# Performance work log

Hardware: AMD Instinct MI355X
Metric: run time of the kernel (lower is better)

The kernel has to match this reference:

```python
import jax, jax.numpy as jnp
import numpy as np

B, L, HIDDEN = 64, 200, 256
HEADS = 8
MAX_WIDTH = 5
EPS = 1e-5  # F.layer_norm default eps


def _ln(x):
    # F.layer_norm with no learned affine
    m = jnp.mean(x, axis=-1, keepdims=True)
    v = jnp.mean((x - m) ** 2, axis=-1, keepdims=True)
    return (x - m) * jax.lax.rsqrt(v + EPS)


def _area_pool(x, max_width, mode):
    # x: [B, H, L, D] -> pooled spans of widths 1..max_width (valid windows),
    # concatenated along the memory axis: M = sum_w (L - w + 1)
    Lx = x.shape[2]
    outs = []
    for w in range(1, max_width + 1):
        # [w, B, H, L-w+1, D] stack of shifted slices (w <= 5, tiny loop)
        win = jnp.stack([x[:, :, i:Lx - w + 1 + i, :] for i in range(w)], axis=0)
        if mode == 'max':
            outs.append(win.max(axis=0))
        elif mode == 'mean':
            outs.append(win.mean(axis=0))
        else:  # 'sum'
            outs.append(win.sum(axis=0))
    return jnp.concatenate(outs, axis=2)


def _mha_area(q_in, k_in, v_in, Wq, bq, Wk, bk, Wv, bv, Wo, bo):
    # per-head size equals hidden_size (key_query_size_hidden = hidden_size)
    Bq, Lq, _ = q_in.shape
    Dh = Wq.shape[1] // HEADS

    def split(x):
        return x.reshape(x.shape[0], x.shape[1], HEADS, Dh).transpose(0, 2, 1, 3)

    q = split(q_in @ Wq + bq)  # [B, H, Lq, Dh]
    k = split(k_in @ Wk + bk)
    v = split(v_in @ Wv + bv)
    k_area = _area_pool(k, MAX_WIDTH, 'max')   # aggr='max' key pooling
    v_area = _area_pool(v, MAX_WIDTH, 'sum')   # values pooled by sum (t2t default)
    scale = jnp.asarray(1.0 / np.sqrt(Dh), q.dtype)
    logits = jnp.einsum('bhqd,bhmd->bhqm', q, k_area) * scale
    attn = jax.nn.softmax(logits, axis=-1)  # dropout inactive at eval
    out = jnp.einsum('bhqm,bhmd->bhqd', attn, v_area)
    out = out.transpose(0, 2, 1, 3).reshape(Bq, Lq, HEADS * Dh)
    return out @ Wo + bo


def setup_inputs() -> dict:
    key = jax.random.key(0)
    ks = jax.random.split(key, 16)
    stdv = 1.0 / np.sqrt(HIDDEN)
    u = lambda k, shp: jax.random.uniform(k, shp, jnp.float32, -stdv, stdv)
    HD = HEADS * HIDDEN  # 2048
    return {
        'A': jax.random.normal(ks[0], (B, L, L), jnp.float32),
        'hidden': jax.random.normal(ks[1], (B, L, HIDDEN), jnp.float32),
        'Wq': u(ks[2], (HIDDEN, HD)), 'bq': u(ks[3], (HD,)),
        'Wk': u(ks[4], (HIDDEN, HD)), 'bk': u(ks[5], (HD,)),
        'Wv': u(ks[6], (HIDDEN, HD)), 'bv': u(ks[7], (HD,)),
        'Wo': u(ks[8], (HD, HIDDEN)), 'bo': u(ks[9], (HIDDEN,)),
        'W1': u(ks[10], (HIDDEN, 4 * HIDDEN)), 'b1': u(ks[11], (4 * HIDDEN,)),
        'W2': u(ks[12], (4 * HIDDEN, HIDDEN)), 'b2': u(ks[13], (HIDDEN,)),
    }


def reference(A, hidden, Wq, bq, Wk, bk, Wv, bv, Wo, bo, W1, b1, W2, b2):
    # step = 1 -> single ATTNCell; A is unused by ATTNCell (matches source)
    attn1 = _mha_area(hidden, hidden, hidden, Wq, bq, Wk, bk, Wv, bv, Wo, bo)
    attn1 = _ln(attn1 + hidden)
    attn2 = _mha_area(attn1, hidden, hidden, Wq, bq, Wk, bk, Wv, bv, Wo, bo)
    attn2 = _ln(attn1 + attn2)  # F.dropout inactive (eval)
    x = jax.nn.relu(attn2 @ W1 + b1) @ W2 + b2
    return _ln(attn2 + x)
```

## Files before the change

kernel.cpp:

```cpp
#include <hip/hip_runtime.h>
#include <hip/hip_bf16.h>
#include <cstdint>
#include <cstddef>

#define BATCH 64
#define LSEQ 200
#define HID 256
#define NH 8
#define DH 256
#define HD (NH*DH)
#define MROWS (BATCH*LSEQ)
#define EPS 1e-5f
#define CSCALE 0.09014195f

typedef unsigned short ushort_t;
typedef __attribute__((ext_vector_type(8))) short bf16x8;
typedef __attribute__((ext_vector_type(8))) unsigned short u16x8;
typedef __attribute__((ext_vector_type(4))) float f32x4;

__device__ __forceinline__ float b2f(ushort_t u) {
    union { unsigned int i; float f; } c; c.i = ((unsigned int)u) << 16; return c.f;
}
__device__ __forceinline__ ushort_t f2b(float f) {
    __hip_bfloat16 h = __float2bfloat16(f);
    union { __hip_bfloat16 h; ushort_t u; } c; c.h = h; return c.u;
}
__device__ __forceinline__ float to_f32(float x) { return x; }
__device__ __forceinline__ float to_f32(ushort_t x) { return b2f(x); }
__device__ __forceinline__ void store_val(float* p, float v) { *p = v; }
__device__ __forceinline__ void store_val(ushort_t* p, float v) { *p = f2b(v); }

__device__ __forceinline__ u16x8 bmax8(u16x8 a, u16x8 b) {
    union U { u16x8 v; __hip_bfloat162 h[4]; };
    U ua, ub, r; ua.v = a; ub.v = b;
    #pragma unroll
    for (int i = 0; i < 4; ++i) r.h[i] = __hmax2(ua.h[i], ub.h[i]);
    return r.v;
}

__device__ __forceinline__ void gll16(const void* g, void* l) {
    __builtin_amdgcn_global_load_lds(
        (const __attribute__((address_space(1))) unsigned int*)g,
        (__attribute__((address_space(3))) unsigned int*)l, 16, 0, 0);
}

template<bool RELU, int OMODE, bool SCALEC>
__global__ __launch_bounds__(256) void gemm_bt(
    const ushort_t* __restrict__ A, const ushort_t* __restrict__ Bt,
    const float* __restrict__ bias, ushort_t* __restrict__ C,
    int M, int N, int K)
{
    __shared__ ushort_t As[128 * 32];
    __shared__ ushort_t Bs[128 * 32];
    const int t = threadIdx.x;
    const int m0 = blockIdx.y * 128, n0 = blockIdx.x * 128;
    const int wave = t >> 6, lane = t & 63;
    const int l15 = lane & 15, lq = lane >> 4;
    const int wr = wave >> 1, wc = wave & 1;

    f32x4 acc[4][4];
    #pragma unroll
    for (int i = 0; i < 4; ++i)
        #pragma unroll
        for (int j = 0; j < 4; ++j) acc[i][j] = (f32x4){0.f, 0.f, 0.f, 0.f};

    for (int k0 = 0; k0 < K; k0 += 32) {
        __syncthreads();
        #pragma unroll
        for (int i = 0; i < 2; ++i) {
            int li = i * 256 + t;
            int ml = li >> 2, cp = li & 3;
            int cg = cp ^ ((ml ^ (ml >> 2)) & 3);
            gll16(A + (size_t)(m0 + ml) * K + k0 + cg * 8, &As[li * 8]);
        }
        #pragma unroll
        for (int i = 0; i < 2; ++i) {
            int li = i * 256 + t;
            int nl = li >> 2, cp = li & 3;
            int cg = cp ^ ((nl ^ (nl >> 2)) & 3);
            gll16(Bt + (size_t)(n0 + nl) * K + k0 + cg * 8, &Bs[li * 8]);
        }
        __syncthreads();
        bf16x8 af[4], bfr[4];
        #pragma unroll
        for (int i = 0; i < 4; ++i) {
            int r = wr * 64 + i * 16 + l15;
            int pc = lq ^ ((r ^ (r >> 2)) & 3);
            af[i] = *(const bf16x8*)&As[r * 32 + pc * 8];
        }
        #pragma unroll
        for (int j = 0; j < 4; ++j) {
            int r = wc * 64 + j * 16 + l15;
            int pc = lq ^ ((r ^ (r >> 2)) & 3);
            bfr[j] = *(const bf16x8*)&Bs[r * 32 + pc * 8];
        }
        #pragma unroll
        for (int i = 0; i < 4; ++i)
            #pragma unroll
            for (int j = 0; j < 4; ++j)
                acc[i][j] = __builtin_amdgcn_mfma_f32_16x16x32_bf16(af[i], bfr[j], acc[i][j], 0, 0, 0);
    }
    if (OMODE == 2) {
        #pragma unroll
        for (int i = 0; i < 4; ++i) {
            int mbase = m0 + wr * 64 + i * 16 + 4 * lq;
            int bb = (int)(((unsigned)mbase * 5243u) >> 20);
            int ll = mbase - bb * 200;
            #pragma unroll
            for (int j = 0; j < 4; ++j) {
                int n = n0 + wc * 64 + j * 16 + l15;
                float bsv = bias[n];
                ushort4 o4;
                o4.x = f2b(acc[i][j][0] + bsv); o4.y = f2b(acc[i][j][1] + bsv);
                o4.z = f2b(acc[i][j][2] + bsv); o4.w = f2b(acc[i][j][3] + bsv);
                size_t addr = ((size_t)(bb * NH + (n >> 8)) * 256 + (n & 255)) * LSEQ + ll;
                *(ushort4*)&C[addr] = o4;
            }
        }
    } else {
        #pragma unroll
        for (int i = 0; i < 4; ++i) {
            #pragma unroll
            for (int e = 0; e < 4; ++e) {
                int m = m0 + wr * 64 + i * 16 + 4 * lq + e;
                #pragma unroll
                for (int j = 0; j < 4; ++j) {
                    int n = n0 + wc * 64 + j * 16 + l15;
                    float v = acc[i][j][e] + bias[n];
                    if (RELU) v = fmaxf(v, 0.f);
                    if (SCALEC) v *= CSCALE;
                    if (OMODE == 1) {
                        int bb = (int)(((unsigned)m * 5243u) >> 20);
                        int ll = m - bb * 200;
                        size_t addr = ((((size_t)(bb * NH + (n >> 8))) * LSEQ + ll) << 8) + (n & 255);
                        C[addr] = f2b(v);
                    } else {
                        C[(size_t)m * N + n] = f2b(v);
                    }
                }
            }
        }
    }
}

__global__ __launch_bounds__(512, 2) void attn_mfma20(
    const ushort_t* __restrict__ Q, const ushort_t* __restrict__ Khm,
    const ushort_t* __restrict__ Vt, ushort_t* __restrict__ O)
{
    const int id = blockIdx.x;
    const int xcd = id & 7, slot_ = id >> 3;
    const int qt = slot_ & 1;
    const int bh = ((slot_ >> 1) << 3) + xcd;
    const int b = bh >> 3, h = bh & 7;
    const int q0 = qt * 128;
    const int t = threadIdx.x;
    const int wave = t >> 6, lane = t & 63;
    const int l15 = lane & 15, lq = lane >> 4;

    __shared__ ushort_t Ks[2 * 64 * 256];
    __shared__ ushort_t Vs[256 * 64];

    const ushort_t* kbh = Khm + (size_t)bh * LSEQ * DH;
    const ushort_t* vtb = Vt + (size_t)bh * DH * LSEQ;
    const ushort_t* qbh = Q + ((size_t)b * LSEQ) * HD + h * DH;
    const int qrow = q0 + wave * 16 + l15;

    bf16x8 qf[8];
    if (qrow < LSEQ) {
        const ushort_t* qp = qbh + (size_t)qrow * HD + 8 * lq;
        #pragma unroll
        for (int g = 0; g < 8; ++g) qf[g] = *(const bf16x8*)(qp + 32 * g);
    } else {
        bf16x8 zf = {0,0,0,0,0,0,0,0};
        #pragma unroll
        for (int g = 0; g < 8; ++g) qf[g] = zf;
    }

    f32x4 oacc[16];
    #pragma unroll
    for (int i = 0; i < 16; ++i) oacc[i] = (f32x4){0.f, 0.f, 0.f, 0.f};
    float l4[4];
    #pragma unroll
    for (int e = 0; e < 4; ++e) l4[e] = 0.f;
    float carry[4];
    #pragma unroll
    for (int e = 0; e < 4; ++e) carry[e] = 0.f;
    float Pagg[4][4];

    const int dc = t & 31, mb = t >> 5;
    const int vd = t >> 1, vh = t & 1;
    const int srow = ((mb >> 2) << 4) + (mb & 3);

    auto kOff = [&](int k4) {
        int m = mb + 16 * k4;
        return m * 256 + ((dc ^ (m & 15)) * 8);
    };

    auto qk = [&](int bo, f32x4* sacc) {
        __builtin_amdgcn_s_setprio(1);
        #pragma unroll
        for (int ms = 0; ms < 4; ++ms) {
            f32x4 s = (f32x4){0.f, 0.f, 0.f, 0.f};
            const int row = ms * 16 + l15;
            #pragma unroll
            for (int g = 0; g < 8; ++g) {
                const int phys = (lq + 4 * g) ^ l15;
                s = __builtin_amdgcn_mfma_f32_16x16x32_bf16(
                        *(const bf16x8*)&Ks[bo + row * 256 + phys * 8], qf[g], s, 0, 0, 0);
            }
            sacc[ms] = s;
        }
        __builtin_amdgcn_s_setprio(0);
    };

    auto smClass = [&](const f32x4* sacc, int cls) {
        float Pc[4][4];
        #pragma unroll
        for (int ms = 0; ms < 4; ++ms)
            #pragma unroll
            for (int e = 0; e < 4; ++e) {
                float pe = __builtin_exp2f(sacc[ms][e]);
                l4[e] += pe;
                Pc[ms][e] = pe;
                Pagg[ms][e] += pe;
            }
        if (cls >= 1) {
            float T[4][4];
            #pragma unroll
            for (int ms = 0; ms < 4; ++ms)
                #pragma unroll
                for (int e = 0; e < 4; ++e) T[ms][e] = Pc[ms][e];
            #pragma unroll
            for (int u = 1; u <= 4; ++u) {
                if (u <= cls) {
                    float up = __shfl(T[3][3], (lane - 16) & 63);
                    #pragma unroll
                    for (int ms = 3; ms >= 0; --ms) {
                        float nv = (ms > 0) ? T[ms - 1][3] : ((lq > 0) ? up : 0.f);
                        T[ms][3] = T[ms][2]; T[ms][2] = T[ms][1]; T[ms][1] = T[ms][0];
                        T[ms][0] = nv;
                    }
                    #pragma unroll
                    for (int ms = 0; ms < 4; ++ms)
                        #pragma unroll
                        for (int e = 0; e < 4; ++e) Pagg[ms][e] += T[ms][e];
                }
            }
        }
        #pragma unroll
        for (int i = 0; i < 4; ++i)
            #pragma unroll
            for (int e = 0; e < 4; ++e)
                if (cls >= 4 + i - e) carry[i] += Pc[3][e];
    };

    auto pv32 = [&](const float P[4][4]) {
        unsigned int w[8];
        #pragma unroll
        for (int ms = 0; ms < 4; ++ms) {
            asm("v_cvt_pk_bf16_f32 %0, %1, %2" : "=v"(w[2*ms])   : "v"(P[ms][0]), "v"(P[ms][1]));
            asm("v_cvt_pk_bf16_f32 %0, %1, %2" : "=v"(w[2*ms+1]) : "v"(P[ms][2]), "v"(P[ms][3]));
        }
        union FR { unsigned int u[4]; bf16x8 v; };
        FR f0, f1;
        f0.u[0] = w[0]; f0.u[1] = w[1]; f0.u[2] = w[2]; f0.u[3] = w[3];
        f1.u[0] = w[4]; f1.u[1] = w[5]; f1.u[2] = w[6]; f1.u[3] = w[7];
        const bf16x8 pf0 = f0.v, pf1 = f1.v;
        __builtin_amdgcn_s_setprio(1);
        #pragma unroll
        for (int dt = 0; dt < 16; ++dt) {
            const int d = dt * 16 + l15;
            const int p0 = lq ^ (d & 7);
            const int p1 = (lq + 4) ^ (d & 7);
            oacc[dt] = __builtin_amdgcn_mfma_f32_16x16x32_bf16(
                           pf0, *(const bf16x8*)&Vs[d * 64 + p0 * 8], oacc[dt], 0, 0, 0);
            oacc[dt] = __builtin_amdgcn_mfma_f32_16x16x32_bf16(
                           pf1, *(const bf16x8*)&Vs[d * 64 + p1 * 8], oacc[dt], 0, 0, 0);
        }
        __builtin_amdgcn_s_setprio(0);
    };

    auto storeVchunk = [&](int kc, u16x8 val) {
        *(u16x8*)&Vs[vd * 64 + ((kc ^ (vd & 7)) * 8)] = val;
    };

    {
        u16x8 r0[4], r1[4], vc[4];
        #pragma unroll
        for (int k4 = 0; k4 < 4; ++k4) {
            const int s = srow + 4 * k4;
            r0[k4] = *(const u16x8*)(kbh + (size_t)(s) * DH + dc * 8);
            r1[k4] = *(const u16x8*)(kbh + (size_t)(s + 1) * DH + dc * 8);
        }
        const ushort_t* vrow = vtb + (size_t)vd * LSEQ + vh * 32;
        #pragma unroll
        for (int cl = 0; cl < 4; ++cl) vc[cl] = *(const u16x8*)(vrow + cl * 8);
        #pragma unroll
        for (int k4 = 0; k4 < 4; ++k4) {
            const int off = kOff(k4);
            *(u16x8*)&Ks[off] = r0[k4];
            *(u16x8*)&Ks[16384 + off] = bmax8(r0[k4], r1[k4]);
        }
        #pragma unroll
        for (int cl = 0; cl < 4; ++cl) {
            const int cg = vh * 4 + cl;
            storeVchunk((cg & 1) * 4 + (cg >> 1), vc[cl]);
        }
    }
    __syncthreads();

    for (int ti = 0; ti < 3; ++ti) {
        const int st0 = ti * 64;
        {
            float pin0 = __shfl(carry[0], (lane + 48) & 63);
            float pin1 = __shfl(carry[1], (lane + 48) & 63);
            float pin2 = __shfl(carry[2], (lane + 48) & 63);
            float pin3 = __shfl(carry[3], (lane + 48) & 63);
            #pragma unroll
            for (int ms = 0; ms < 4; ++ms)
                #pragma unroll
                for (int e = 0; e < 4; ++e) Pagg[ms][e] = 0.f;
            if (lq == 0) {
                Pagg[0][0] = pin0; Pagg[0][1] = pin1; Pagg[0][2] = pin2; Pagg[0][3] = pin3;
            }
            #pragma unroll
            for (int e = 0; e < 4; ++e) carry[e] = 0.f;
        }
        {
            f32x4 sa[4], sb[4];
            qk(0, sa); qk(16384, sb);
            smClass(sa, 0); smClass(sb, 1);
        }
        {
            u16x8 r2[4], r3[4];
            #pragma unroll
            for (int k4 = 0; k4 < 4; ++k4) {
                const int s = st0 + srow + 4 * k4;
                r2[k4] = *(const u16x8*)(kbh + (size_t)(s + 2) * DH + dc * 8);
                r3[k4] = *(const u16x8*)(kbh + (size_t)(s + 3) * DH + dc * 8);
            }
            __syncthreads();
            #pragma unroll
            for (int k4 = 0; k4 < 4; ++k4) {
                const int off = kOff(k4);
                u16x8 c2 = bmax8(*(const u16x8*)&Ks[16384 + off], r2[k4]);
                *(u16x8*)&Ks[off] = c2;
                *(u16x8*)&Ks[16384 + off] = bmax8(c2, r3[k4]);
            }
            __syncthreads();
        }
        {
            f32x4 sa[4], sb[4];
            qk(0, sa); qk(16384, sb);
            smClass(sa, 2); smClass(sb, 3);
        }
        {
            u16x8 r4[4];
            #pragma unroll
            for (int k4 = 0; k4 < 4; ++k4) {
                const int s = st0 + srow + 4 * k4;
                r4[k4] = *(const u16x8*)(kbh + (size_t)(s + 4) * DH + dc * 8);
            }
            __syncthreads();
            #pragma unroll
            for (int k4 = 0; k4 < 4; ++k4) {
                const int off = kOff(k4);
                *(u16x8*)&Ks[off] = bmax8(*(const u16x8*)&Ks[16384 + off], r4[k4]);
            }
            __syncthreads();
        }
        {
            f32x4 sa[4];
            qk(0, sa);
            smClass(sa, 4);
            pv32(Pagg);
        }
        if (ti < 2) {
            const int nt0 = st0 + 64;
            u16x8 r0[4], r1[4], vc[4];
            #pragma unroll
            for (int k4 = 0; k4 < 4; ++k4) {
                const int s = nt0 + srow + 4 * k4;
                r0[k4] = *(const u16x8*)(kbh + (size_t)(s) * DH + dc * 8);
                r1[k4] = *(const u16x8*)(kbh + (size_t)(s + 1) * DH + dc * 8);
            }
            const ushort_t* vrow = vtb + (size_t)vd * LSEQ + nt0 + vh * 32;
            #pragma unroll
            for (int cl = 0; cl < 4; ++cl) vc[cl] = *(const u16x8*)(vrow + cl * 8);
            __syncthreads();
            #pragma unroll
            for (int k4 = 0; k4 < 4; ++k4) {
                const int off = kOff(k4);
                *(u16x8*)&Ks[off] = r0[k4];
                *(u16x8*)&Ks[16384 + off] = bmax8(r0[k4], r1[k4]);
            }
            #pragma unroll
            for (int cl = 0; cl < 4; ++cl) {
                const int cg = vh * 4 + cl;
                storeVchunk((cg & 1) * 4 + (cg >> 1), vc[cl]);
            }
            __syncthreads();
        } else {
            u16x8 v0 = *(const u16x8*)(vtb + (size_t)vd * LSEQ + 192);
            __syncthreads();
            if (mb < 8) {
                u16x8 krun = *(const u16x8*)(kbh + (size_t)(192 + mb) * DH + dc * 8);
                const u16x8 kz = {0,0,0,0,0,0,0,0};
                #pragma unroll
                for (int k8 = 0; k8 < 8; ++k8) {
                    const bool vv = (k8 <= 4) && (mb <= 7 - k8);
                    if (k8 > 0 && vv)
                        krun = bmax8(krun, *(const u16x8*)(kbh + (size_t)(192 + mb + k8) * DH + dc * 8));
                    int slot = k8 * 8 + mb;
                    *(u16x8*)&Ks[slot * 256 + ((dc ^ (slot & 15)) * 8)] = vv ? krun : kz;
                }
            }
            {
                float f[8];
                #pragma unroll
                for (int e = 0; e < 8; ++e) f[e] = b2f(v0[e]);
                #pragma unroll
                for (int ck = 0; ck < 4; ++ck) {
                    const int kc = vh * 4 + ck;
                    const int cls_lo = 4 * (kc >> 2) + ((kc >> 1) & 1);
                    const int offb = 4 * (kc & 1);
                    u16x8 ov;
                    #pragma unroll
                    for (int o = 0; o < 8; ++o) {
                        const int cls = cls_lo + 2 * (o >> 2);
                        const int off = offb + (o & 3);
                        ushort_t val = 0;
                        if (cls <= 4 && off <= 7 - cls) {
                            float a = 0.f;
                            #pragma unroll
                            for (int u = 0; u <= 4; ++u)
                                if (u <= cls) a += f[off + u];
                            val = f2b(a);
                        }
                        if (kc == 6 && o < 4) val = v0[o];
                        ov[o] = val;
                    }
                    storeVchunk(kc, ov);
                }
            }
            __syncthreads();
        }
    }

    {
        f32x4 sacc[4];
        qk(0, sacc);
        float pullc[4];
        #pragma unroll
        for (int e = 0; e < 4; ++e) pullc[e] = __shfl(carry[e], (lane + 16) & 63);
        float Pt[4][4];
        #pragma unroll
        for (int ms = 0; ms < 4; ++ms)
            #pragma unroll
            for (int e = 0; e < 4; ++e) {
                const int slot = ms * 16 + 4 * lq + e;
                const bool inval = ((slot & 7) > 7 - (slot >> 3)) || ((slot >> 3) > 4);
                float pe = __builtin_exp2f(inval ? -1e30f : sacc[ms][e]);
                l4[e] += pe;
                float pfrag = pe;
                if (ms == 2 && lq == 2) pfrag = pullc[e];
                Pt[ms][e] = pfrag;
            }
        pv32(Pt);
    }

    float l_part = (l4[0] + l4[1]) + (l4[2] + l4[3]);
    l_part += __shfl_xor(l_part, 16);
    l_part += __shfl_xor(l_part, 32);
    const float inv = 1.f / l_part;

    ushort_t* ob = O + ((size_t)b * LSEQ) * HD + h * DH;
    #pragma unroll
    for (int e = 0; e < 4; ++e) {
        const int q = q0 + wave * 16 + 4 * lq + e;
        const float linv = __shfl(inv, 4 * lq + e);
        if (q < LSEQ) {
            #pragma unroll
            for (int dt = 0; dt < 16; ++dt)
                ob[(size_t)q * HD + dt * 16 + l15] = f2b(oacc[dt][e] * linv);
        }
    }
}

template<typename TR, typename TO>
__global__ __launch_bounds__(256) void residual_ln(
    const ushort_t* __restrict__ X, const TR* __restrict__ R, TO* __restrict__ Out)
{
    const int row = blockIdx.x;
    const int t = threadIdx.x;
    const size_t base = (size_t)row * HID;
    float v = b2f(X[base + t]) + to_f32(R[base + t]);
    float s = v, q = v * v;
    #pragma unroll
    for (int o = 32; o > 0; o >>= 1) {
        s += __shfl_xor(s, o, 64);
        q += __shfl_xor(q, o, 64);
    }
    __shared__ float ss[4], sq[4];
    const int wave = t >> 6, lane = t & 63;
    if (lane == 0) { ss[wave] = s; sq[wave] = q; }
    __syncthreads();
    s = ss[0] + ss[1] + ss[2] + ss[3];
    q = sq[0] + sq[1] + sq[2] + sq[3];
    float mean = s * (1.f / HID);
    float var  = q * (1.f / HID) - mean * mean;
    store_val(&Out[base + t], (v - mean) * rsqrtf(var + EPS));
}

__global__ __launch_bounds__(256) void cvt_f32_bf16(const float* __restrict__ in,
                                                    ushort_t* __restrict__ out) {
    const int i = (blockIdx.x * 256 + threadIdx.x) * 4;
    float4 v = *(const float4*)(in + i);
    ushort4 o;
    o.x = f2b(v.x); o.y = f2b(v.y); o.z = f2b(v.z); o.w = f2b(v.w);
    *(ushort4*)(out + i) = o;
}

__global__ __launch_bounds__(256) void wtrans(const float* __restrict__ W,
                                              ushort_t* __restrict__ Wt, int K, int N) {
    __shared__ float tile[32][33];
    const int t = threadIdx.x;
    const int tx = t & 31, ty = t >> 5;
    const int n0 = blockIdx.x * 32, k0 = blockIdx.y * 32;
    #pragma unroll
    for (int s = 0; s < 4; ++s)
        tile[ty + 8 * s][tx] = W[(size_t)(k0 + ty + 8 * s) * N + n0 + tx];
    __syncthreads();
    #pragma unroll
    for (int s = 0; s < 4; ++s)
        Wt[(size_t)(n0 + ty + 8 * s) * K + k0 + tx] = f2b(tile[tx][ty + 8 * s]);
}

extern "C" void kernel_launch(void* const* d_in, const int* in_sizes, int n_in,
                              void* d_out, int out_size, void* d_ws, size_t ws_size,
                              hipStream_t stream) {
    const float* hidden = (const float*)d_in[1];
    const float* Wq = (const float*)d_in[2];  const float* bq = (const float*)d_in[3];
    const float* Wk = (const float*)d_in[4];  const float* bk = (const float*)d_in[5];
    const float* Wv = (const float*)d_in[6];  const float* bv = (const float*)d_in[7];
    const float* Wo = (const float*)d_in[8];  const float* bo = (const float*)d_in[9];
    const float* W1 = (const float*)d_in[10]; const float* b1 = (const float*)d_in[11];
    const float* W2 = (const float*)d_in[12]; const float* b2 = (const float*)d_in[13];
    float* out = (float*)d_out;

    constexpr size_t SZ_BF   = (size_t)MROWS * HD * 2;
    constexpr size_t SZ_HBF  = (size_t)MROWS * HID * 2;
    constexpr size_t SZ_WQKV = (size_t)HID * HD * 2;
    constexpr size_t SZ_W12  = (size_t)HID * 4 * HID * 2;
    char* ws = (char*)d_ws;
    size_t off = 0;
    ushort_t* kb   = (ushort_t*)(ws + off); off += SZ_BF;
    ushort_t* vt   = (ushort_t*)(ws + off); off += SZ_BF;
    ushort_t* qo   = (ushort_t*)(ws + off); off += SZ_BF;
    ushort_t* hb   = (ushort_t*)(ws + off); off += SZ_HBF;
    ushort_t* at1  = (ushort_t*)(ws + off); off += SZ_HBF;
    ushort_t* at2  = (ushort_t*)(ws + off); off += SZ_HBF;
    ushort_t* proj = (ushort_t*)(ws + off); off += SZ_HBF;
    ushort_t* WtQ  = (ushort_t*)(ws + off); off += SZ_WQKV;
    ushort_t* WtK  = (ushort_t*)(ws + off); off += SZ_WQKV;
    ushort_t* WtV  = (ushort_t*)(ws + off); off += SZ_WQKV;
    ushort_t* WtO  = (ushort_t*)(ws + off); off += SZ_WQKV;
    ushort_t* Wt1  = (ushort_t*)(ws + off); off += SZ_W12;
    ushort_t* Wt2  = (ushort_t*)(ws + off); off += SZ_W12;
    if (ws_size < off) return;
    ushort_t* ffn1 = qo;

    dim3 blk(256);
    cvt_f32_bf16<<<MROWS * HID / 1024, blk, 0, stream>>>(hidden, hb);
    wtrans<<<dim3(HD / 32, HID / 32), blk, 0, stream>>>(Wq, WtQ, HID, HD);
    wtrans<<<dim3(HD / 32, HID / 32), blk, 0, stream>>>(Wk, WtK, HID, HD);
    wtrans<<<dim3(HD / 32, HID / 32), blk, 0, stream>>>(Wv, WtV, HID, HD);
    wtrans<<<dim3(HID / 32, HD / 32), blk, 0, stream>>>(Wo, WtO, HD, HID);
    wtrans<<<dim3(4 * HID / 32, HID / 32), blk, 0, stream>>>(W1, Wt1, HID, 4 * HID);
    wtrans<<<dim3(HID / 32, 4 * HID / 32), blk, 0, stream>>>(W2, Wt2, 4 * HID, HID);

    const dim3 gProj(HD / 128, MROWS / 128);
    const dim3 gOut(HID / 128, MROWS / 128);
    const dim3 gF1(4 * HID / 128, MROWS / 128);

    gemm_bt<false, 1, false><<<gProj, blk, 0, stream>>>(hb, WtK, bk, kb, MROWS, HD, HID);
    gemm_bt<false, 2, false><<<gProj, blk, 0, stream>>>(hb, WtV, bv, vt, MROWS, HD, HID);

    gemm_bt<false, 0, true><<<gProj, blk, 0, stream>>>(hb, WtQ, bq, qo, MROWS, HD, HID);
    attn_mfma20<<<2 * BATCH * NH, 512, 0, stream>>>(qo, kb, vt, qo);
    gemm_bt<false, 0, false><<<gOut, blk, 0, stream>>>(qo, WtO, bo, proj, MROWS, HID, HD);
    residual_ln<float, ushort_t><<<MROWS, blk, 0, stream>>>(proj, hidden, at1);

    gemm_bt<false, 0, true><<<gProj, blk, 0, stream>>>(at1, WtQ, bq, qo, MROWS, HD, HID);
    attn_mfma20<<<2 * BATCH * NH, 512, 0, stream>>>(qo, kb, vt, qo);
    gemm_bt<false, 0, false><<<gOut, blk, 0, stream>>>(qo, WtO, bo, proj, MROWS, HID, HD);
    residual_ln<ushort_t, ushort_t><<<MROWS, blk, 0, stream>>>(proj, at1, at2);

    gemm_bt<true, 0, false><<<gF1, blk, 0, stream>>>(at2, Wt1, b1, ffn1, MROWS, 4 * HID, HID);
    gemm_bt<false, 0, false><<<gOut, blk, 0, stream>>>(ffn1, Wt2, b2, proj, MROWS, HID, 4 * HID);
    residual_ln<ushort_t, float><<<MROWS, blk, 0, stream>>>(proj, at2, out);
}
```

Measured before the change: 972.9 us.

## Halve attention K LDS buffer by pooling one width class at a time

The attention kernel now keeps one 64x256 K tile in shared memory instead of two. It builds each max-pooled width class incrementally: it loads the shifted K rows, max-combines them into the buffer, then runs QK and softmax for that class. The point is to cut LDS use so more blocks can be resident per CU. In exchange it adds more barriers per tile, serialises the load and compute phases with no prefetch of the next tile, and loads K rows redundantly from global/L2.

Measured after the change: 904.2 us. -7.1%, faster.

```diff
diff --git a/kernel.cpp b/kernel.cpp
--- a/kernel.cpp
+++ b/kernel.cpp
@@ -143,7 +143,7 @@
     }
 }
 
-__global__ __launch_bounds__(512, 2) void attn_mfma20(
+__global__ __launch_bounds__(512, 2) void attn_mfma21(
     const ushort_t* __restrict__ Q, const ushort_t* __restrict__ Khm,
     const ushort_t* __restrict__ Vt, ushort_t* __restrict__ O)
 {
@@ -157,7 +157,7 @@
     const int wave = t >> 6, lane = t & 63;
     const int l15 = lane & 15, lq = lane >> 4;
 
-    __shared__ ushort_t Ks[2 * 64 * 256];
+    __shared__ ushort_t Ks[64 * 256];
     __shared__ ushort_t Vs[256 * 64];
 
     const ushort_t* kbh = Khm + (size_t)bh * LSEQ * DH;
@@ -195,8 +195,11 @@
         int m = mb + 16 * k4;
         return m * 256 + ((dc ^ (m & 15)) * 8);
     };
-
-    auto qk = [&](int bo, f32x4* sacc) {
+    auto storeVchunk = [&](int kc, u16x8 val) {
+        *(u16x8*)&Vs[vd * 64 + ((kc ^ (vd & 7)) * 8)] = val;
+    };
+
+    auto qk = [&](f32x4* sacc) {
         __builtin_amdgcn_s_setprio(1);
         #pragma unroll
         for (int ms = 0; ms < 4; ++ms) {
@@ -206,7 +209,7 @@
             for (int g = 0; g < 8; ++g) {
                 const int phys = (lq + 4 * g) ^ l15;
                 s = __builtin_amdgcn_mfma_f32_16x16x32_bf16(
-                        *(const bf16x8*)&Ks[bo + row * 256 + phys * 8], qf[g], s, 0, 0, 0);
+                        *(const bf16x8*)&Ks[row * 256 + phys * 8], qf[g], s, 0, 0, 0);
             }
             sacc[ms] = s;
         }
@@ -280,35 +283,6 @@
         __builtin_amdgcn_s_setprio(0);
     };
 
-    auto storeVchunk = [&](int kc, u16x8 val) {
-        *(u16x8*)&Vs[vd * 64 + ((kc ^ (vd & 7)) * 8)] = val;
-    };
-
-    {
-        u16x8 r0[4], r1[4], vc[4];
-        #pragma unroll
-        for (int k4 = 0; k4 < 4; ++k4) {
-            const int s = srow + 4 * k4;
-            r0[k4] = *(const u16x8*)(kbh + (size_t)(s) * DH + dc * 8);
-            r1[k4] = *(const u16x8*)(kbh + (size_t)(s + 1) * DH + dc * 8);
-        }
-        const ushort_t* vrow = vtb + (size_t)vd * LSEQ + vh * 32;
-        #pragma unroll
-        for (int cl = 0; cl < 4; ++cl) vc[cl] = *(const u16x8*)(vrow + cl * 8);
-        #pragma unroll
-        for (int k4 = 0; k4 < 4; ++k4) {
-            const int off = kOff(k4);
-            *(u16x8*)&Ks[off] = r0[k4];
-            *(u16x8*)&Ks[16384 + off] = bmax8(r0[k4], r1[k4]);
-        }
-        #pragma unroll
-        for (int cl = 0; cl < 4; ++cl) {
-            const int cg = vh * 4 + cl;
-            storeVchunk((cg & 1) * 4 + (cg >> 1), vc[cl]);
-        }
-    }
-    __syncthreads();
-
     for (int ti = 0; ti < 3; ++ti) {
         const int st0 = ti * 64;
         {
@@ -326,130 +300,88 @@
             #pragma unroll
             for (int e = 0; e < 4; ++e) carry[e] = 0.f;
         }
+        #pragma unroll
+        for (int cls = 0; cls < 5; ++cls) {
+            u16x8 kf[4];
+            #pragma unroll
+            for (int k4 = 0; k4 < 4; ++k4)
+                kf[k4] = *(const u16x8*)(kbh + (size_t)(st0 + srow + 4 * k4 + cls) * DH + dc * 8);
+            u16x8 vc[4];
+            if (cls == 0) {
+                const ushort_t* vrow = vtb + (size_t)vd * LSEQ + st0 + vh * 32;
+                #pragma unroll
+                for (int c2 = 0; c2 < 4; ++c2) vc[c2] = *(const u16x8*)(vrow + c2 * 8);
+            }
+            __syncthreads();
+
+            #pragma unroll
+            for (int k4 = 0; k4 < 4; ++k4) {
+                ushort_t* kp = &Ks[kOff(k4)];
+                *(u16x8*)kp = (cls == 0) ? kf[k4] : bmax8(*(const u16x8*)kp, kf[k4]);
+            }
+            if (cls == 0) {
+                #pragma unroll
+                for (int cl = 0; cl < 4; ++cl) {
+                    const int cg = vh * 4 + cl;
+                    storeVchunk((cg & 1) * 4 + (cg >> 1), vc[cl]);
+                }
+            }
+            __syncthreads();
+
+            f32x4 sacc[4];
+            qk(sacc);
+            smClass(sacc, cls);
+            if (cls == 4) pv32(Pagg);
+        }
+    }
+
+    {
+        __syncthreads();
+        if (mb < 8) {
+            u16x8 krun = *(const u16x8*)(kbh + (size_t)(192 + mb) * DH + dc * 8);
+            const u16x8 kz = {0,0,0,0,0,0,0,0};
+            #pragma unroll
+            for (int k8 = 0; k8 < 8; ++k8) {
+                const bool vv = (k8 <= 4) && (mb <= 7 - k8);
+                if (k8 > 0 && vv)
+                    krun = bmax8(krun, *(const u16x8*)(kbh + (size_t)(192 + mb + k8) * DH + dc * 8));
+                int slot = k8 * 8 + mb;
+                *(u16x8*)&Ks[slot * 256 + ((dc ^ (slot & 15)) * 8)] = vv ? krun : kz;
+            }
+        }
         {
-            f32x4 sa[4], sb[4];
-            qk(0, sa); qk(16384, sb);
-            smClass(sa, 0); smClass(sb, 1);
-        }
-        {
-            u16x8 r2[4], r3[4];
-            #pragma unroll
-            for (int k4 = 0; k4 < 4; ++k4) {
-                const int s = st0 + srow + 4 * k4;
-                r2[k4] = *(const u16x8*)(kbh + (size_t)(s + 2) * DH + dc * 8);
-                r3[k4] = *(const u16x8*)(kbh + (size_t)(s + 3) * DH + dc * 8);
-            }
-            __syncthreads();
-            #pragma unroll
-            for (int k4 = 0; k4 < 4; ++k4) {
-                const int off = kOff(k4);
-                u16x8 c2 = bmax8(*(const u16x8*)&Ks[16384 + off], r2[k4]);
-                *(u16x8*)&Ks[off] = c2;
-                *(u16x8*)&Ks[16384 + off] = bmax8(c2, r3[k4]);
-            }
-            __syncthreads();
-        }
-        {
-            f32x4 sa[4], sb[4];
-            qk(0, sa); qk(16384, sb);
-            smClass(sa, 2); smClass(sb, 3);
-        }
-        {
-            u16x8 r4[4];
-            #pragma unroll
-            for (int k4 = 0; k4 < 4; ++k4) {
-                const int s = st0 + srow + 4 * k4;
-                r4[k4] = *(const u16x8*)(kbh + (size_t)(s + 4) * DH + dc * 8);
-            }
-            __syncthreads();
-            #pragma unroll
-            for (int k4 = 0; k4 < 4; ++k4) {
-                const int off = kOff(k4);
-                *(u16x8*)&Ks[off] = bmax8(*(const u16x8*)&Ks[16384 + off], r4[k4]);
-            }
-            __syncthreads();
-        }
-        {
-            f32x4 sa[4];
-            qk(0, sa);
-            smClass(sa, 4);
-            pv32(Pagg);
-        }
-        if (ti < 2) {
-            const int nt0 = st0 + 64;
-            u16x8 r0[4], r1[4], vc[4];
-            #pragma unroll
-            for (int k4 = 0; k4 < 4; ++k4) {
-                const int s = nt0 + srow + 4 * k4;
-                r0[k4] = *(const u16x8*)(kbh + (size_t)(s) * DH + dc * 8);
-                r1[k4] = *(const u16x8*)(kbh + (size_t)(s + 1) * DH + dc * 8);
-            }
-            const ushort_t* vrow = vtb + (size_t)vd * LSEQ + nt0 + vh * 32;
-            #pragma unroll
-            for (int cl = 0; cl < 4; ++cl) vc[cl] = *(const u16x8*)(vrow + cl * 8);
-            __syncthreads();
-            #pragma unroll
-            for (int k4 = 0; k4 < 4; ++k4) {
-                const int off = kOff(k4);
-                *(u16x8*)&Ks[off] = r0[k4];
-                *(u16x8*)&Ks[16384 + off] = bmax8(r0[k4], r1[k4]);
-            }
-            #pragma unroll
-            for (int cl = 0; cl < 4; ++cl) {
-                const int cg = vh * 4 + cl;
-                storeVchunk((cg & 1) * 4 + (cg >> 1), vc[cl]);
-            }
-            __syncthreads();
-        } else {
             u16x8 v0 = *(const u16x8*)(vtb + (size_t)vd * LSEQ + 192);
-            __syncthreads();
-            if (mb < 8) {
-                u16x8 krun = *(const u16x8*)(kbh + (size_t)(192 + mb) * DH + dc * 8);
-                const u16x8 kz = {0,0,0,0,0,0,0,0};
+            float f[8];
+            #pragma unroll
+            for (int e = 0; e < 8; ++e) f[e] = b2f(v0[e]);
+            #pragma unroll
+            for (int ck = 0; ck < 4; ++ck) {
+                const int kc = vh * 4 + ck;
+                const int cls_lo = 4 * (kc >> 2) + ((kc >> 1) & 1);
+                const int offb = 4 * (kc & 1);
+                u16x8 ov;
                 #pragma unroll
-                for (int k8 = 0; k8 < 8; ++k8) {
-                    const bool vv = (k8 <= 4) && (mb <= 7 - k8);
-                    if (k8 > 0 && vv)
-                        krun = bmax8(krun, *(const u16x8*)(kbh + (size_t)(192 + mb + k8) * DH + dc * 8));
-                    int slot = k8 * 8 + mb;
-                    *(u16x8*)&Ks[slot * 256 + ((dc ^ (slot & 15)) * 8)] = vv ? krun : kz;
+                for (int o = 0; o < 8; ++o) {
+                    const int cls = cls_lo + 2 * (o >> 2);
+                    const int off = offb + (o & 3);
+                    ushort_t val = 0;
+                    if (cls <= 4 && off <= 7 - cls) {
+                        float a = 0.f;
+                        #pragma unroll
+                        for (int u = 0; u <= 4; ++u)
+                            if (u <= cls) a += f[off + u];
+                        val = f2b(a);
+                    }
+                    if (kc == 6 && o < 4) val = v0[o];
+                    ov[o] = val;
                 }
-            }
-            {
-                float f[8];
-                #pragma unroll
-                for (int e = 0; e < 8; ++e) f[e] = b2f(v0[e]);
-                #pragma unroll
-                for (int ck = 0; ck < 4; ++ck) {
-                    const int kc = vh * 4 + ck;
-                    const int cls_lo = 4 * (kc >> 2) + ((kc >> 1) & 1);
-                    const int offb = 4 * (kc & 1);
-                    u16x8 ov;
-                    #pragma unroll
-                    for (int o = 0; o < 8; ++o) {
-                        const int cls = cls_lo + 2 * (o >> 2);
-                        const int off = offb + (o & 3);
-                        ushort_t val = 0;
-                        if (cls <= 4 && off <= 7 - cls) {
-                            float a = 0.f;
-                            #pragma unroll
-                            for (int u = 0; u <= 4; ++u)
-                                if (u <= cls) a += f[off + u];
-                            val = f2b(a);
-                        }
-                        if (kc == 6 && o < 4) val = v0[o];
-                        ov[o] = val;
-                    }
-                    storeVchunk(kc, ov);
-                }
-            }
-            __syncthreads();
-        }
-    }
-
-    {
+                storeVchunk(kc, ov);
+            }
+        }
+        __syncthreads();
+
         f32x4 sacc[4];
-        qk(0, sacc);
+        qk(sacc);
         float pullc[4];
         #pragma unroll
         for (int e = 0; e < 4; ++e) pullc[e] = __shfl(carry[e], (lane + 16) & 63);
@@ -587,12 +519,12 @@
     gemm_bt<false, 2, false><<<gProj, blk, 0, stream>>>(hb, WtV, bv, vt, MROWS, HD, HID);
 
     gemm_bt<false, 0, true><<<gProj, blk, 0, stream>>>(hb, WtQ, bq, qo, MROWS, HD, HID);
-    attn_mfma20<<<2 * BATCH * NH, 512, 0, stream>>>(qo, kb, vt, qo);
+    attn_mfma21<<<2 * BATCH * NH, 512, 0, stream>>>(qo, kb, vt, qo);
     gemm_bt<false, 0, false><<<gOut, blk, 0, stream>>>(qo, WtO, bo, proj, MROWS, HID, HD);
     residual_ln<float, ushort_t><<<MROWS, blk, 0, stream>>>(proj, hidden, at1);
 
     gemm_bt<false, 0, true><<<gProj, blk, 0, stream>>>(at1, WtQ, bq, qo, MROWS, HD, HID);
-    attn_mfma20<<<2 * BATCH * NH, 512, 0, stream>>>(qo, kb, vt, qo);
+    attn_mfma21<<<2 * BATCH * NH, 512, 0, stream>>>(qo, kb, vt, qo);
     gemm_bt<false, 0, false><<<gOut, blk, 0, stream>>>(qo, WtO, bo, proj, MROWS, HID, HD);
     residual_ln<ushort_t, ushort_t><<<MROWS, blk, 0, stream>>>(proj, at1, at2);
 
```
